# Performance work log

Measured on AMD Instinct MI355X. Metric: run time of the kernel, lower is better.

## Reference

```python
import jax, jax.numpy as jnp
import numpy as np

H = 1024
EPS = 1e-5
N_ENT = 1000
TOP_K = 5


def _ln(x, g, b):
    mu = jnp.mean(x, axis=-1, keepdims=True)
    var = jnp.mean((x - mu) ** 2, axis=-1, keepdims=True)
    return (x - mu) * jax.lax.rsqrt(var + EPS) * g + b


def _gelu(x):
    return jax.nn.gelu(x, approximate=False)  # torch nn.GELU default (erf)


def setup_inputs() -> dict:
    key = jax.random.key(0)
    ks = jax.random.split(key, 24)
    s = 0.02
    inp = {
        'hidden_states': jax.random.normal(ks[0], (8, 2048, H), jnp.float32),
        'entity_embeddings': jax.random.normal(ks[1], (N_ENT, H), jnp.float32) * 0.01,
        # entity_encoder: H -> 2H -> H -> LN
        'ee_w1': jax.random.normal(ks[2], (H, 2 * H), jnp.float32) * s,
        'ee_b1': jnp.zeros((2 * H,), jnp.float32),
        'ee_w2': jax.random.normal(ks[3], (2 * H, H), jnp.float32) * s,
        'ee_b2': jnp.zeros((H,), jnp.float32),
        'ee_g': jnp.ones((H,), jnp.float32),
        'ee_beta': jnp.zeros((H,), jnp.float32),
        # relation_encoder: H -> H -> H -> LN
        're_w1': jax.random.normal(ks[4], (H, H), jnp.float32) * s,
        're_b1': jnp.zeros((H,), jnp.float32),
        're_w2': jax.random.normal(ks[5], (H, H), jnp.float32) * s,
        're_b2': jnp.zeros((H,), jnp.float32),
        're_g': jnp.ones((H,), jnp.float32),
        're_beta': jnp.zeros((H,), jnp.float32),
        # reasoning_network: 3H -> 2H -> H -> LN
        'rn_w1': jax.random.normal(ks[6], (3 * H, 2 * H), jnp.float32) * s,
        'rn_b1': jnp.zeros((2 * H,), jnp.float32),
        'rn_w2': jax.random.normal(ks[7], (2 * H, H), jnp.float32) * s,
        'rn_b2': jnp.zeros((H,), jnp.float32),
        'rn_g': jnp.ones((H,), jnp.float32),
        'rn_beta': jnp.zeros((H,), jnp.float32),
        # validation_network: H -> H/2 -> 1 -> sigmoid
        'vn_w1': jax.random.normal(ks[8], (H, H // 2), jnp.float32) * s,
        'vn_b1': jnp.zeros((H // 2,), jnp.float32),
        'vn_w2': jax.random.normal(ks[9], (H // 2, 1), jnp.float32) * s,
        'vn_b2': jnp.zeros((1,), jnp.float32),
    }
    return inp


def reference(hidden_states, entity_embeddings,
              ee_w1, ee_b1, ee_w2, ee_b2, ee_g, ee_beta,
              re_w1, re_b1, re_w2, re_b2, re_g, re_beta,
              rn_w1, rn_b1, rn_w2, rn_b2, rn_g, rn_beta,
              vn_w1, vn_b1, vn_w2, vn_b2):
    # entity encoder over all tokens: [B,S,H]
    entity_features = _ln(_gelu(hidden_states @ ee_w1 + ee_b1) @ ee_w2 + ee_b2, ee_g, ee_beta)

    # query=None path: relation encoder on mean-pooled hidden states [B,H]
    pooled = jnp.mean(hidden_states, axis=1)
    relation_features = _ln(_gelu(pooled @ re_w1 + re_b1) @ re_w2 + re_b2, re_g, re_beta)
    query_features = relation_features

    # similarity + top-k entity retrieval
    entity_similarities = query_features @ entity_embeddings.T  # [B, N_ENT]
    top_values, top_indices = jax.lax.top_k(entity_similarities, TOP_K)
    retrieved_entities = entity_embeddings[top_indices]  # [B, K, H]

    # reasoning input: [mean retrieved entity | relation | mean context]
    entity_vec = jnp.mean(retrieved_entities, axis=1)  # [B,H]
    context_vec = jnp.mean(hidden_states, axis=1)      # [B,H]
    reasoning_in = jnp.concatenate([entity_vec, relation_features, context_vec], axis=-1)  # [B,3H]
    reasoning_output = _ln(_gelu(reasoning_in @ rn_w1 + rn_b1) @ rn_w2 + rn_b2, rn_g, rn_beta)

    validation_scores = jax.nn.sigmoid(_gelu(reasoning_output @ vn_w1 + vn_b1) @ vn_w2 + vn_b2)

    return (entity_features, relation_features, retrieved_entities,
            entity_similarities, top_indices, reasoning_output, validation_scores)
```

## Files before the change

### kernel.cpp

```cpp
#include <hip/hip_runtime.h>
#include <math.h>

#define H 1024
#define SEQ 2048
#define BATCH 8
#define N_ENT 1000
#define TOPK 5
#define LN_EPS 1e-5f

using bf16x8 = __attribute__((ext_vector_type(8))) __bf16;
using f32x4  = __attribute__((ext_vector_type(4))) float;
#define AS1 __attribute__((address_space(1)))
#define AS3 __attribute__((address_space(3)))


__device__ __forceinline__ float gelu_fast(float x) {
    float z = fabsf(x) * 0.70710678118654752440f;
    float t = __builtin_amdgcn_rcpf(fmaf(0.3275911f, z, 1.0f));
    float p = fmaf(fmaf(fmaf(fmaf(1.061405429f, t, -1.453152027f), t, 1.421413741f),
                        t, -0.284496736f), t, 0.254829592f) * t;
    float e = __builtin_amdgcn_exp2f(-z * z * 1.44269504088896f);
    float erfz = fmaf(-p, e, 1.0f);
    float s = copysignf(erfz, x);
    return 0.5f * x * (1.0f + s);
}

__device__ __forceinline__ float sigmoidf_(float x) {
    return 1.0f / (1.0f + expf(-x));
}

__device__ __forceinline__ unsigned short f2bf(float f) {
    unsigned int u = __float_as_uint(f);
    unsigned int r = (u + 0x7fffu + ((u >> 16) & 1u)) >> 16;
    return (unsigned short)r;
}

__device__ float block_sum(float v, float* red) {
    for (int off = 32; off > 0; off >>= 1) v += __shfl_down(v, off, 64);
    int wid = threadIdx.x >> 6;
    int lane = threadIdx.x & 63;
    int nw = blockDim.x >> 6;
    if (lane == 0) red[wid] = v;
    __syncthreads();
    if (threadIdx.x == 0) {
        float s = 0.f;
        for (int i = 0; i < nw; ++i) s += red[i];
        red[0] = s;
    }
    __syncthreads();
    float r = red[0];
    __syncthreads();
    return r;
}


__global__ void f2bf_kernel(const float* __restrict__ in, unsigned short* __restrict__ out, int n) {
    int i = (blockIdx.x * blockDim.x + threadIdx.x) * 4;
    if (i >= n) return;
    float4 v = *(const float4*)(in + i);
    ushort4 o;
    o.x = f2bf(v.x); o.y = f2bf(v.y); o.z = f2bf(v.z); o.w = f2bf(v.w);
    *(ushort4*)(out + i) = o;
}

__global__ void transpose_bf_kernel(const float* __restrict__ in, unsigned short* __restrict__ out,
                                    int R, int C) {
    __shared__ float tile[32][33];
    int c0 = blockIdx.x * 32, r0 = blockIdx.y * 32;
    int tx = threadIdx.x & 31, ty = threadIdx.x >> 5;
#pragma unroll
    for (int i = 0; i < 32; i += 8)
        tile[ty + i][tx] = in[(size_t)(r0 + ty + i) * C + c0 + tx];
    __syncthreads();
#pragma unroll
    for (int i = 0; i < 32; i += 8)
        out[(size_t)(c0 + ty + i) * R + r0 + tx] = f2bf(tile[tx][ty + i]);
}


__global__ void pool1_kernel(const float* __restrict__ hs, float* __restrict__ part,
                             unsigned short* __restrict__ hsb) {
    int sc = blockIdx.x, b = blockIdx.y, t = threadIdx.x;
    float a0 = 0, a1 = 0, a2 = 0, a3 = 0;
    size_t rowbase = (size_t)b * SEQ + sc * 64;
    const float* p = hs + rowbase * H;
    for (int s = 0; s < 64; ++s) {
        const float* q = p + (size_t)s * H;
        float v0 = q[t], v1 = q[t + 256], v2 = q[t + 512], v3 = q[t + 768];
        a0 += v0; a1 += v1; a2 += v2; a3 += v3;
        if (hsb) {
            unsigned short* w = hsb + (rowbase + s) * H;
            w[t] = f2bf(v0); w[t + 256] = f2bf(v1); w[t + 512] = f2bf(v2); w[t + 768] = f2bf(v3);
        }
    }
    float* o = part + ((size_t)b * 32 + sc) * H;
    o[t] = a0; o[t + 256] = a1; o[t + 512] = a2; o[t + 768] = a3;
}

__global__ void pool2_kernel(const float* __restrict__ part, float* __restrict__ pooled) {
    int b = blockIdx.y, c = blockIdx.x, t = threadIdx.x;
    float s = 0.f;
    for (int sc = 0; sc < 32; ++sc) s += part[((size_t)b * 32 + sc) * H + t + c * 256];
    pooled[b * H + t + c * 256] = s * (1.0f / SEQ);
}


template <int KRANGE>
__global__ void mlp_partial_kernel(const float* __restrict__ X, int ldx,
                                   const float* __restrict__ W, int N,
                                   float* __restrict__ part) {
    __shared__ float xs[8][KRANGE];
    int jb = blockIdx.x, ks = blockIdx.y, t = threadIdx.x;
    int k0 = ks * KRANGE;
    for (int i = t; i < 8 * KRANGE; i += 256) {
        int b = i / KRANGE, k = i % KRANGE;
        xs[b][k] = X[(size_t)b * ldx + k0 + k];
    }
    __syncthreads();
    int j = jb * 256 + t;
    float acc[8] = {};
    for (int k = 0; k < KRANGE; ++k) {
        float w = W[(size_t)(k0 + k) * N + j];
#pragma unroll
        for (int b = 0; b < 8; ++b) acc[b] = fmaf(xs[b][k], w, acc[b]);
    }
#pragma unroll
    for (int b = 0; b < 8; ++b) part[((size_t)ks * 8 + b) * N + j] = acc[b];
}

__global__ void mlp_reduce_gelu_kernel(const float* __restrict__ part, const float* __restrict__ bias,
                                       float* __restrict__ out, int N, int nks) {
    int b = blockIdx.y;
    int j = blockIdx.x * 256 + threadIdx.x;
    float s = bias[j];
    for (int ks = 0; ks < nks; ++ks) s += part[((size_t)ks * 8 + b) * N + j];
    out[(size_t)b * N + j] = gelu_fast(s);
}

__global__ void mlp_reduce_ln_kernel(const float* __restrict__ part, const float* __restrict__ bias,
                                     const float* __restrict__ g, const float* __restrict__ be,
                                     float* __restrict__ out, int nks) {
    __shared__ float red[32];
    int b = blockIdx.x, t = threadIdx.x;
    float s = bias[t];
    for (int ks = 0; ks < nks; ++ks) s += part[((size_t)ks * 8 + b) * H + t];
    float mu = block_sum(s, red) * (1.0f / H);
    float d = s - mu;
    float var = block_sum(d * d, red) * (1.0f / H);
    out[(size_t)b * H + t] = d * rsqrtf(var + LN_EPS) * g[t] + be[t];
}


__global__ void sim_kernel(const float* __restrict__ rel, const float* __restrict__ ent,
                           float* __restrict__ sims) {
    __shared__ float rl[8 * H];
    int t = threadIdx.x;
    for (int i = t; i < 8 * H; i += 256) rl[i] = rel[i];
    __syncthreads();
    int e = blockIdx.x * 4 + (t >> 6);
    int lane = t & 63;
    float ev[16];
    const float* ep = ent + (size_t)e * H;
#pragma unroll
    for (int i = 0; i < 16; ++i) ev[i] = ep[lane + i * 64];
#pragma unroll
    for (int b = 0; b < 8; ++b) {
        float a = 0.f;
#pragma unroll
        for (int i = 0; i < 16; ++i) a = fmaf(ev[i], rl[b * H + lane + i * 64], a);
        for (int off = 32; off > 0; off >>= 1) a += __shfl_down(a, off, 64);
        if (lane == 0) sims[b * N_ENT + e] = a;
    }
}

__global__ void topk_kernel(const float* __restrict__ sims, float* __restrict__ out_idx_f,
                            int* __restrict__ idx_i) {
    __shared__ float v[1024];
    __shared__ float rv[4];
    __shared__ int ri[4];
    int b = blockIdx.x, t = threadIdx.x;
    for (int i = t; i < 1024; i += 256) v[i] = (i < N_ENT) ? sims[b * N_ENT + i] : -INFINITY;
    __syncthreads();
    for (int k = 0; k < TOPK; ++k) {
        float best = -INFINITY;
        int bi = 0x7fffffff;
        for (int i = t; i < 1024; i += 256) {
            float x = v[i];
            if (x > best || (x == best && i < bi)) { best = x; bi = i; }
        }
        for (int off = 32; off > 0; off >>= 1) {
            float ov = __shfl_down(best, off, 64);
            int oi = __shfl_down(bi, off, 64);
            if (ov > best || (ov == best && oi < bi)) { best = ov; bi = oi; }
        }
        if ((t & 63) == 0) { rv[t >> 6] = best; ri[t >> 6] = bi; }
        __syncthreads();
        if (t == 0) {
            for (int w = 1; w < 4; ++w)
                if (rv[w] > rv[0] || (rv[w] == rv[0] && ri[w] < ri[0])) { rv[0] = rv[w]; ri[0] = ri[w]; }
            int sel = ri[0];
            out_idx_f[b * TOPK + k] = (float)sel;
            idx_i[b * TOPK + k] = sel;
            v[sel] = -INFINITY;
        }
        __syncthreads();
    }
}

__global__ void gather_concat_kernel(const float* __restrict__ ent, const int* __restrict__ idx,
                                     const float* __restrict__ rel, const float* __restrict__ pooled,
                                     float* __restrict__ retrieved, float* __restrict__ xin) {
    int b = blockIdx.x, h = threadIdx.x;
    float acc = 0.f;
    for (int k = 0; k < TOPK; ++k) {
        float v = ent[(size_t)idx[b * TOPK + k] * H + h];
        retrieved[((size_t)b * TOPK + k) * H + h] = v;
        acc += v;
    }
    float* xb = xin + (size_t)b * 3 * H;
    xb[h] = acc * (1.0f / TOPK);
    xb[H + h] = rel[b * H + h];
    xb[2 * H + h] = pooled[b * H + h];
}

__global__ void vn_final_kernel(const float* __restrict__ part, const float* __restrict__ b1,
                                const float* __restrict__ w2, const float* __restrict__ b2,
                                float* __restrict__ vs, int nks) {
    __shared__ float red[32];
    int b = blockIdx.x, t = threadIdx.x;
    float s = b1[t];
    for (int ks = 0; ks < nks; ++ks) s += part[((size_t)ks * 8 + b) * 512 + t];
    float c = gelu_fast(s) * w2[t];
    float tot = block_sum(c, red);
    if (t == 0) vs[b] = sigmoidf_(tot + b2[0]);
}

template <int GELU_BF16_OUT>
__global__ __launch_bounds__(256) void gemm_mfma(const unsigned short* __restrict__ A,
                                                 const unsigned short* __restrict__ Bt,
                                                 const float* __restrict__ bias,
                                                 void* __restrict__ Cout,
                                                 int M, int N, int K) {
    __shared__ __align__(16) unsigned short As[128 * 32];
    __shared__ __align__(16) unsigned short Bs[128 * 32];
    const int tid = threadIdx.x;
    const int lane = tid & 63;
    const int Mp = M >> 7;
    const int m0 = (blockIdx.x % Mp) * 128;
    const int n0 = (blockIdx.x / Mp) * 128;
    const int wave = tid >> 6;
    const int wm = (wave >> 1) * 64, wn = (wave & 1) * 64;

    const int rowA_f = wm + (lane & 15);
    const int rowB_f = wn + (lane & 15);
    const int kq = (lane >> 4) * 8;

    f32x4 acc[4][4] = {};

    for (int k0 = 0; k0 < K; k0 += 32) {
#pragma unroll
        for (int r = 0; r < 2; ++r) {
            int e = (r * 256 + tid) * 8;
            int row = e >> 5, kk = e & 31;
            const unsigned short* ga = A + (size_t)(m0 + row) * K + k0 + kk;
            const unsigned short* gb = Bt + (size_t)(n0 + row) * K + k0 + kk;
            unsigned short* la = As + (size_t)(r * 256 + (tid & ~63)) * 8;
            unsigned short* lb = Bs + (size_t)(r * 256 + (tid & ~63)) * 8;
            __builtin_amdgcn_global_load_lds((AS1 void*)ga, (AS3 void*)la, 16, 0, 0);
            __builtin_amdgcn_global_load_lds((AS1 void*)gb, (AS3 void*)lb, 16, 0, 0);
        }
        __syncthreads();
        bf16x8 af[4], bfg[4];
#pragma unroll
        for (int i = 0; i < 4; ++i)
            af[i] = *(const bf16x8*)(As + (rowA_f + i * 16) * 32 + kq);
#pragma unroll
        for (int j = 0; j < 4; ++j)
            bfg[j] = *(const bf16x8*)(Bs + (rowB_f + j * 16) * 32 + kq);
#pragma unroll
        for (int i = 0; i < 4; ++i)
#pragma unroll
            for (int j = 0; j < 4; ++j)
                acc[i][j] = __builtin_amdgcn_mfma_f32_16x16x32_bf16(af[i], bfg[j], acc[i][j], 0, 0, 0);
        __syncthreads();
    }

    const int cn = lane & 15;
    const int rbase = (lane >> 4) * 4;
#pragma unroll
    for (int i = 0; i < 4; ++i) {
#pragma unroll
        for (int j = 0; j < 4; ++j) {
            int n = n0 + wn + j * 16 + cn;
            float bv = bias[n];
            int mb = m0 + wm + i * 16 + rbase;
#pragma unroll
            for (int r = 0; r < 4; ++r) {
                float c = acc[i][j][r] + bv;
                if (GELU_BF16_OUT) {
                    c = gelu_fast(c);
                    ((unsigned short*)Cout)[(size_t)(mb + r) * N + n] = f2bf(c);
                } else {
                    ((float*)Cout)[(size_t)(mb + r) * N + n] = c;
                }
            }
        }
    }
}

__global__ void ln_rows_kernel(float* __restrict__ x, const float* __restrict__ g,
                               const float* __restrict__ beta) {
    __shared__ float red[32];
    float* p = x + (size_t)blockIdx.x * H;
    int t = threadIdx.x;
    float4 v = *(const float4*)(p + t * 4);
    float s = v.x + v.y + v.z + v.w;
    float mu = block_sum(s, red) * (1.0f / H);
    float4 d = { v.x - mu, v.y - mu, v.z - mu, v.w - mu };
    float d2 = d.x * d.x + d.y * d.y + d.z * d.z + d.w * d.w;
    float var = block_sum(d2, red) * (1.0f / H);
    float inv = rsqrtf(var + LN_EPS);
    float4 gg = *(const float4*)(g + t * 4);
    float4 bb = *(const float4*)(beta + t * 4);
    float4 o = { d.x * inv * gg.x + bb.x, d.y * inv * gg.y + bb.y,
                 d.z * inv * gg.z + bb.z, d.w * inv * gg.w + bb.w };
    *(float4*)(p + t * 4) = o;
}


extern "C" void kernel_launch(void* const* d_in, const int* in_sizes, int n_in,
                              void* d_out, int out_size, void* d_ws, size_t ws_size,
                              hipStream_t stream) {
    const float* hs     = (const float*)d_in[0];
    const float* ent    = (const float*)d_in[1];
    const float* ee_w1  = (const float*)d_in[2];
    const float* ee_b1  = (const float*)d_in[3];
    const float* ee_w2  = (const float*)d_in[4];
    const float* ee_b2  = (const float*)d_in[5];
    const float* ee_g   = (const float*)d_in[6];
    const float* ee_be  = (const float*)d_in[7];
    const float* re_w1  = (const float*)d_in[8];
    const float* re_b1  = (const float*)d_in[9];
    const float* re_w2  = (const float*)d_in[10];
    const float* re_b2  = (const float*)d_in[11];
    const float* re_g   = (const float*)d_in[12];
    const float* re_be  = (const float*)d_in[13];
    const float* rn_w1  = (const float*)d_in[14];
    const float* rn_b1  = (const float*)d_in[15];
    const float* rn_w2  = (const float*)d_in[16];
    const float* rn_b2  = (const float*)d_in[17];
    const float* rn_g   = (const float*)d_in[18];
    const float* rn_be  = (const float*)d_in[19];
    const float* vn_w1  = (const float*)d_in[20];
    const float* vn_b1  = (const float*)d_in[21];
    const float* vn_w2  = (const float*)d_in[22];
    const float* vn_b2  = (const float*)d_in[23];

    float* out = (float*)d_out;
    float* ef   = out;
    float* rel  = ef + (size_t)BATCH * SEQ * H;
    float* retr = rel + BATCH * H;
    float* sims = retr + BATCH * TOPK * H;
    float* tidx = sims + BATCH * N_ENT;
    float* ro   = tidx + BATCH * TOPK;
    float* vs   = ro + BATCH * H;

    float* ws = (float*)d_ws;
    size_t o = 0;
    float* pooled = ws + o; o += 8192;
    int*   idx_i  = (int*)(ws + o); o += 64;
    float* xin    = ws + o; o += 8 * 3 * H;
    float* h1r    = ws + o; o += 8 * H;
    float* h1n    = ws + o; o += 8 * 2 * H;
    float* part   = ws + o; o += 24 * 8 * 2048;
    unsigned short* w1t = (unsigned short*)(ws + o); o += (2048 * 1024) / 2;
    unsigned short* w2t = (unsigned short*)(ws + o); o += (2048 * 1024) / 2;
    unsigned short* hsb = (unsigned short*)(ws + o);

    long long avail = (long long)(ws_size / 4) - (long long)o;
    int chunk = (int)(avail / 1536);
    chunk &= ~127;
    int total = BATCH * SEQ;
    if (chunk > total) chunk = total;
    if (chunk < 128) chunk = 128;
    bool full = (chunk >= total);
    unsigned short* midb = hsb + (size_t)chunk * H;

    transpose_bf_kernel<<<dim3(2048 / 32, 1024 / 32), 256, 0, stream>>>(ee_w1, w1t, 1024, 2048);
    transpose_bf_kernel<<<dim3(1024 / 32, 2048 / 32), 256, 0, stream>>>(ee_w2, w2t, 2048, 1024);

    pool1_kernel<<<dim3(32, BATCH), 256, 0, stream>>>(hs, part, full ? hsb : nullptr);
    pool2_kernel<<<dim3(4, BATCH), 256, 0, stream>>>(part, pooled);

    mlp_partial_kernel<64><<<dim3(4, 16), 256, 0, stream>>>(pooled, H, re_w1, H, part);
    mlp_reduce_gelu_kernel<<<dim3(4, 8), 256, 0, stream>>>(part, re_b1, h1r, H, 16);
    mlp_partial_kernel<64><<<dim3(4, 16), 256, 0, stream>>>(h1r, H, re_w2, H, part);
    mlp_reduce_ln_kernel<<<BATCH, 1024, 0, stream>>>(part, re_b2, re_g, re_be, rel, 16);

    sim_kernel<<<250, 256, 0, stream>>>(rel, ent, sims);
    topk_kernel<<<BATCH, 256, 0, stream>>>(sims, tidx, idx_i);
    gather_concat_kernel<<<BATCH, 1024, 0, stream>>>(ent, idx_i, rel, pooled, retr, xin);

    mlp_partial_kernel<128><<<dim3(8, 24), 256, 0, stream>>>(xin, 3 * H, rn_w1, 2 * H, part);
    mlp_reduce_gelu_kernel<<<dim3(8, 8), 256, 0, stream>>>(part, rn_b1, h1n, 2 * H, 24);
    mlp_partial_kernel<128><<<dim3(4, 16), 256, 0, stream>>>(h1n, 2 * H, rn_w2, H, part);
    mlp_reduce_ln_kernel<<<BATCH, 1024, 0, stream>>>(part, rn_b2, rn_g, rn_be, ro, 16);

    mlp_partial_kernel<128><<<dim3(2, 8), 256, 0, stream>>>(ro, H, vn_w1, 512, part);
    vn_final_kernel<<<BATCH, 512, 0, stream>>>(part, vn_b1, vn_w2, vn_b2, vs, 8);

    for (int r0 = 0; r0 < total; r0 += chunk) {
        int m = total - r0;
        if (m > chunk) m = chunk;
        if (!full) {
            int nconv = m * H;
            f2bf_kernel<<<(nconv / 4 + 255) / 256, 256, 0, stream>>>(hs + (size_t)r0 * H, hsb, nconv);
        }
        unsigned short* a1 = full ? (hsb + (size_t)r0 * H) : hsb;
        gemm_mfma<1><<<(m / 128) * (2048 / 128), 256, 0, stream>>>(a1, w1t, ee_b1, midb,
                                                                   m, 2048, 1024);
        gemm_mfma<0><<<(m / 128) * (1024 / 128), 256, 0, stream>>>(midb, w2t, ee_b2,
                                                                   ef + (size_t)r0 * H,
                                                                   m, 1024, 2048);
    }
    ln_rows_kernel<<<total, 256, 0, stream>>>(ef, ee_g, ee_be);
}
```

Before: 617.7 us.

## Double-buffer MFMA GEMM LDS tiles, group tile order, fuse small MLP reductions

The bf16 MFMA GEMM now keeps two LDS buffers, so the next K-slice is loaded while MFMAs run on the current one, with one barrier per iteration instead of two. Output tiles are also ordered in groups of 8 M-tiles to improve L2 reuse of the weight tiles. Separately, the small batch-8 MLPs drop the split-K partial-plus-reduce kernels for a single fc_kernel that reduces within the block and applies bias and GELU directly. This cuts launches and partial-buffer traffic, but far fewer blocks stream the large weight matrices, which may lower bandwidth on those layers.

```diff
diff --git a/kernel.cpp b/kernel.cpp
--- a/kernel.cpp
+++ b/kernel.cpp
@@ -104,46 +104,45 @@
     pooled[b * H + t + c * 256] = s * (1.0f / SEQ);
 }
 
-
-template <int KRANGE>
-__global__ void mlp_partial_kernel(const float* __restrict__ X, int ldx,
-                                   const float* __restrict__ W, int N,
-                                   float* __restrict__ part) {
-    __shared__ float xs[8][KRANGE];
-    int jb = blockIdx.x, ks = blockIdx.y, t = threadIdx.x;
-    int k0 = ks * KRANGE;
-    for (int i = t; i < 8 * KRANGE; i += 256) {
-        int b = i / KRANGE, k = i % KRANGE;
-        xs[b][k] = X[(size_t)b * ldx + k0 + k];
-    }
-    __syncthreads();
-    int j = jb * 256 + t;
+template <int K, int ACT>
+__global__ __launch_bounds__(256) void fc_kernel(const float* __restrict__ X,
+                                                 const float* __restrict__ W,
+                                                 const float* __restrict__ bias, int N,
+                                                 float* __restrict__ out) {
+    __shared__ float xs[8 * K];
+    __shared__ float red[4][8][64];
+    int t = threadIdx.x;
+    for (int i = t; i < 8 * K; i += 256) xs[i] = X[i];
+    __syncthreads();
+    int cl = t & 63;
+    int c = blockIdx.x * 64 + cl;
+    int s = t >> 6;
+    const int KS = K / 4;
     float acc[8] = {};
-    for (int k = 0; k < KRANGE; ++k) {
-        float w = W[(size_t)(k0 + k) * N + j];
-#pragma unroll
-        for (int b = 0; b < 8; ++b) acc[b] = fmaf(xs[b][k], w, acc[b]);
-    }
-#pragma unroll
-    for (int b = 0; b < 8; ++b) part[((size_t)ks * 8 + b) * N + j] = acc[b];
-}
-
-__global__ void mlp_reduce_gelu_kernel(const float* __restrict__ part, const float* __restrict__ bias,
-                                       float* __restrict__ out, int N, int nks) {
-    int b = blockIdx.y;
-    int j = blockIdx.x * 256 + threadIdx.x;
-    float s = bias[j];
-    for (int ks = 0; ks < nks; ++ks) s += part[((size_t)ks * 8 + b) * N + j];
-    out[(size_t)b * N + j] = gelu_fast(s);
-}
-
-__global__ void mlp_reduce_ln_kernel(const float* __restrict__ part, const float* __restrict__ bias,
-                                     const float* __restrict__ g, const float* __restrict__ be,
-                                     float* __restrict__ out, int nks) {
+#pragma unroll 4
+    for (int k = s * KS; k < (s + 1) * KS; ++k) {
+        float w = W[(size_t)k * N + c];
+#pragma unroll
+        for (int b = 0; b < 8; ++b) acc[b] = fmaf(xs[b * K + k], w, acc[b]);
+    }
+#pragma unroll
+    for (int b = 0; b < 8; ++b) red[s][b][cl] = acc[b];
+    __syncthreads();
+    if (s == 0) {
+#pragma unroll
+        for (int b = 0; b < 8; ++b) {
+            float v = red[0][b][cl] + red[1][b][cl] + red[2][b][cl] + red[3][b][cl] + bias[c];
+            if (ACT) v = gelu_fast(v);
+            out[(size_t)b * N + c] = v;
+        }
+    }
+}
+
+__global__ void ln_vec_kernel(const float* __restrict__ in, const float* __restrict__ g,
+                              const float* __restrict__ be, float* __restrict__ out) {
     __shared__ float red[32];
     int b = blockIdx.x, t = threadIdx.x;
-    float s = bias[t];
-    for (int ks = 0; ks < nks; ++ks) s += part[((size_t)ks * 8 + b) * H + t];
+    float s = in[(size_t)b * H + t];
     float mu = block_sum(s, red) * (1.0f / H);
     float d = s - mu;
     float var = block_sum(d * d, red) * (1.0f / H);
@@ -223,14 +222,11 @@
     xb[2 * H + h] = pooled[b * H + h];
 }
 
-__global__ void vn_final_kernel(const float* __restrict__ part, const float* __restrict__ b1,
-                                const float* __restrict__ w2, const float* __restrict__ b2,
-                                float* __restrict__ vs, int nks) {
+__global__ void vn_final_kernel(const float* __restrict__ h, const float* __restrict__ w2,
+                                const float* __restrict__ b2, float* __restrict__ vs) {
     __shared__ float red[32];
     int b = blockIdx.x, t = threadIdx.x;
-    float s = b1[t];
-    for (int ks = 0; ks < nks; ++ks) s += part[((size_t)ks * 8 + b) * 512 + t];
-    float c = gelu_fast(s) * w2[t];
+    float c = h[(size_t)b * 512 + t] * w2[t];
     float tot = block_sum(c, red);
     if (t == 0) vs[b] = sigmoidf_(tot + b2[0]);
 }
@@ -241,48 +237,62 @@
                                                  const float* __restrict__ bias,
                                                  void* __restrict__ Cout,
                                                  int M, int N, int K) {
-    __shared__ __align__(16) unsigned short As[128 * 32];
-    __shared__ __align__(16) unsigned short Bs[128 * 32];
+    __shared__ __align__(16) unsigned short As[2][128 * 32];
+    __shared__ __align__(16) unsigned short Bs[2][128 * 32];
     const int tid = threadIdx.x;
     const int lane = tid & 63;
-    const int Mp = M >> 7;
-    const int m0 = (blockIdx.x % Mp) * 128;
-    const int n0 = (blockIdx.x / Mp) * 128;
+
+    const int Mp = M >> 7, Np = N >> 7;
+    const int GM = 8;
+    int per_group = GM * Np;
+    int group = blockIdx.x / per_group;
+    int rem = blockIdx.x - group * per_group;
+    int gbase = group * GM;
+    int gm = Mp - gbase; if (gm > GM) gm = GM;
+    const int m0 = (gbase + rem % gm) * 128;
+    const int n0 = (rem / gm) * 128;
+
     const int wave = tid >> 6;
     const int wm = (wave >> 1) * 64, wn = (wave & 1) * 64;
-
     const int rowA_f = wm + (lane & 15);
     const int rowB_f = wn + (lane & 15);
     const int kq = (lane >> 4) * 8;
 
-    f32x4 acc[4][4] = {};
-
-    for (int k0 = 0; k0 < K; k0 += 32) {
+    auto stage = [&](int kbase, int buf) {
 #pragma unroll
         for (int r = 0; r < 2; ++r) {
             int e = (r * 256 + tid) * 8;
             int row = e >> 5, kk = e & 31;
-            const unsigned short* ga = A + (size_t)(m0 + row) * K + k0 + kk;
-            const unsigned short* gb = Bt + (size_t)(n0 + row) * K + k0 + kk;
-            unsigned short* la = As + (size_t)(r * 256 + (tid & ~63)) * 8;
-            unsigned short* lb = Bs + (size_t)(r * 256 + (tid & ~63)) * 8;
+            const unsigned short* ga = A + (size_t)(m0 + row) * K + kbase + kk;
+            const unsigned short* gb = Bt + (size_t)(n0 + row) * K + kbase + kk;
+            unsigned short* la = &As[buf][(size_t)(r * 256 + (tid & ~63)) * 8];
+            unsigned short* lb = &Bs[buf][(size_t)(r * 256 + (tid & ~63)) * 8];
             __builtin_amdgcn_global_load_lds((AS1 void*)ga, (AS3 void*)la, 16, 0, 0);
             __builtin_amdgcn_global_load_lds((AS1 void*)gb, (AS3 void*)lb, 16, 0, 0);
         }
+    };
+
+    f32x4 acc[4][4] = {};
+    stage(0, 0);
+    int cur = 0;
+    for (int k0 = 0; k0 < K; k0 += 32) {
         __syncthreads();
+        if (k0 + 32 < K) stage(k0 + 32, cur ^ 1);
+        const unsigned short* Ab = As[cur];
+        const unsigned short* Bb = Bs[cur];
         bf16x8 af[4], bfg[4];
 #pragma unroll
         for (int i = 0; i < 4; ++i)
-            af[i] = *(const bf16x8*)(As + (rowA_f + i * 16) * 32 + kq);
+            af[i] = *(const bf16x8*)(Ab + (rowA_f + i * 16) * 32 + kq);
 #pragma unroll
         for (int j = 0; j < 4; ++j)
-            bfg[j] = *(const bf16x8*)(Bs + (rowB_f + j * 16) * 32 + kq);
+            bfg[j] = *(const bf16x8*)(Bb + (rowB_f + j * 16) * 32 + kq);
 #pragma unroll
         for (int i = 0; i < 4; ++i)
 #pragma unroll
             for (int j = 0; j < 4; ++j)
                 acc[i][j] = __builtin_amdgcn_mfma_f32_16x16x32_bf16(af[i], bfg[j], acc[i][j], 0, 0, 0);
-        __syncthreads();
+        cur ^= 1;
     }
 
     const int cn = lane & 15;
@@ -371,8 +381,11 @@
     int*   idx_i  = (int*)(ws + o); o += 64;
     float* xin    = ws + o; o += 8 * 3 * H;
     float* h1r    = ws + o; o += 8 * H;
+    float* relp   = ws + o; o += 8 * H;
     float* h1n    = ws + o; o += 8 * 2 * H;
-    float* part   = ws + o; o += 24 * 8 * 2048;
+    float* rop    = ws + o; o += 8 * H;
+    float* h1v    = ws + o; o += 8 * 512;
+    float* part   = ws + o; o += 8 * 32 * H;
     unsigned short* w1t = (unsigned short*)(ws + o); o += (2048 * 1024) / 2;
     unsigned short* w2t = (unsigned short*)(ws + o); o += (2048 * 1024) / 2;
     unsigned short* hsb = (unsigned short*)(ws + o);
@@ -392,22 +405,20 @@
     pool1_kernel<<<dim3(32, BATCH), 256, 0, stream>>>(hs, part, full ? hsb : nullptr);
     pool2_kernel<<<dim3(4, BATCH), 256, 0, stream>>>(part, pooled);
 
-    mlp_partial_kernel<64><<<dim3(4, 16), 256, 0, stream>>>(pooled, H, re_w1, H, part);
-    mlp_reduce_gelu_kernel<<<dim3(4, 8), 256, 0, stream>>>(part, re_b1, h1r, H, 16);
-    mlp_partial_kernel<64><<<dim3(4, 16), 256, 0, stream>>>(h1r, H, re_w2, H, part);
-    mlp_reduce_ln_kernel<<<BATCH, 1024, 0, stream>>>(part, re_b2, re_g, re_be, rel, 16);
+    fc_kernel<1024, 1><<<16, 256, 0, stream>>>(pooled, re_w1, re_b1, 1024, h1r);
+    fc_kernel<1024, 0><<<16, 256, 0, stream>>>(h1r, re_w2, re_b2, 1024, relp);
+    ln_vec_kernel<<<BATCH, 1024, 0, stream>>>(relp, re_g, re_be, rel);
 
     sim_kernel<<<250, 256, 0, stream>>>(rel, ent, sims);
     topk_kernel<<<BATCH, 256, 0, stream>>>(sims, tidx, idx_i);
     gather_concat_kernel<<<BATCH, 1024, 0, stream>>>(ent, idx_i, rel, pooled, retr, xin);
 
-    mlp_partial_kernel<128><<<dim3(8, 24), 256, 0, stream>>>(xin, 3 * H, rn_w1, 2 * H, part);
-    mlp_reduce_gelu_kernel<<<dim3(8, 8), 256, 0, stream>>>(part, rn_b1, h1n, 2 * H, 24);
-    mlp_partial_kernel<128><<<dim3(4, 16), 256, 0, stream>>>(h1n, 2 * H, rn_w2, H, part);
-    mlp_reduce_ln_kernel<<<BATCH, 1024, 0, stream>>>(part, rn_b2, rn_g, rn_be, ro, 16);
-
-    mlp_partial_kernel<128><<<dim3(2, 8), 256, 0, stream>>>(ro, H, vn_w1, 512, part);
-    vn_final_kernel<<<BATCH, 512, 0, stream>>>(part, vn_b1, vn_w2, vn_b2, vs, 8);
+    fc_kernel<3072, 1><<<32, 256, 0, stream>>>(xin, rn_w1, rn_b1, 2048, h1n);
+    fc_kernel<2048, 0><<<16, 256, 0, stream>>>(h1n, rn_w2, rn_b2, 1024, rop);
+    ln_vec_kernel<<<BATCH, 1024, 0, stream>>>(rop, rn_g, rn_be, ro);
+
+    fc_kernel<1024, 1><<<8, 256, 0, stream>>>(ro, vn_w1, vn_b1, 512, h1v);
+    vn_final_kernel<<<BATCH, 512, 0, stream>>>(h1v, vn_w2, vn_b2, vs);
 
     for (int r0 = 0; r0 < total; r0 += chunk) {
         int m = total - r0;
```

Measured after the change: 753.5 us. 1.22x slower.

## Double-buffer GEMM LDS tiles, add grouped block swizzle, vectorize pooling

Applied to the files above, without the earlier changes.

The MFMA GEMM now keeps two LDS buffers and issues the next K-tile's global-to-LDS loads before computing the current tile. This drops one barrier per iteration and overlaps memory with MFMA work. Blocks are remapped into groups of 8 M-tiles for better L2 reuse of B tiles. The pooling kernels switch to float4 loads and stores, and pool2 now launches one block per batch. The risks are twice the LDS per block, which can lower occupancy, and a possible race, since a single barrier per iteration may let the next prefetch overwrite a buffer other waves are still reading.

```diff
diff --git a/kernel.cpp b/kernel.cpp
--- a/kernel.cpp
+++ b/kernel.cpp
@@ -81,27 +81,30 @@
 __global__ void pool1_kernel(const float* __restrict__ hs, float* __restrict__ part,
                              unsigned short* __restrict__ hsb) {
     int sc = blockIdx.x, b = blockIdx.y, t = threadIdx.x;
-    float a0 = 0, a1 = 0, a2 = 0, a3 = 0;
     size_t rowbase = (size_t)b * SEQ + sc * 64;
-    const float* p = hs + rowbase * H;
+    const float* p = hs + rowbase * H + t * 4;
+    float4 a = {0.f, 0.f, 0.f, 0.f};
     for (int s = 0; s < 64; ++s) {
-        const float* q = p + (size_t)s * H;
-        float v0 = q[t], v1 = q[t + 256], v2 = q[t + 512], v3 = q[t + 768];
-        a0 += v0; a1 += v1; a2 += v2; a3 += v3;
+        float4 v = *(const float4*)(p + (size_t)s * H);
+        a.x += v.x; a.y += v.y; a.z += v.z; a.w += v.w;
         if (hsb) {
-            unsigned short* w = hsb + (rowbase + s) * H;
-            w[t] = f2bf(v0); w[t + 256] = f2bf(v1); w[t + 512] = f2bf(v2); w[t + 768] = f2bf(v3);
-        }
-    }
-    float* o = part + ((size_t)b * 32 + sc) * H;
-    o[t] = a0; o[t + 256] = a1; o[t + 512] = a2; o[t + 768] = a3;
+            ushort4 o;
+            o.x = f2bf(v.x); o.y = f2bf(v.y); o.z = f2bf(v.z); o.w = f2bf(v.w);
+            *(ushort4*)(hsb + (rowbase + s) * H + t * 4) = o;
+        }
+    }
+    *(float4*)(part + ((size_t)b * 32 + sc) * H + t * 4) = a;
 }
 
 __global__ void pool2_kernel(const float* __restrict__ part, float* __restrict__ pooled) {
-    int b = blockIdx.y, c = blockIdx.x, t = threadIdx.x;
-    float s = 0.f;
-    for (int sc = 0; sc < 32; ++sc) s += part[((size_t)b * 32 + sc) * H + t + c * 256];
-    pooled[b * H + t + c * 256] = s * (1.0f / SEQ);
+    int b = blockIdx.x, t = threadIdx.x;
+    float4 s = {0.f, 0.f, 0.f, 0.f};
+    for (int sc = 0; sc < 32; ++sc) {
+        float4 v = *(const float4*)(part + ((size_t)b * 32 + sc) * H + t * 4);
+        s.x += v.x; s.y += v.y; s.z += v.z; s.w += v.w;
+    }
+    float4 o = {s.x * (1.0f / SEQ), s.y * (1.0f / SEQ), s.z * (1.0f / SEQ), s.w * (1.0f / SEQ)};
+    *(float4*)(pooled + (size_t)b * H + t * 4) = o;
 }
 
 
@@ -241,48 +244,62 @@
                                                  const float* __restrict__ bias,
                                                  void* __restrict__ Cout,
                                                  int M, int N, int K) {
-    __shared__ __align__(16) unsigned short As[128 * 32];
-    __shared__ __align__(16) unsigned short Bs[128 * 32];
+    __shared__ __align__(16) unsigned short As[2][128 * 32];
+    __shared__ __align__(16) unsigned short Bs[2][128 * 32];
     const int tid = threadIdx.x;
     const int lane = tid & 63;
-    const int Mp = M >> 7;
-    const int m0 = (blockIdx.x % Mp) * 128;
-    const int n0 = (blockIdx.x / Mp) * 128;
+
+    const int Mp = M >> 7, Np = N >> 7;
+    const int GM = 8;
+    int per_group = GM * Np;
+    int group = blockIdx.x / per_group;
+    int rem = blockIdx.x - group * per_group;
+    int gbase = group * GM;
+    int gm = Mp - gbase; if (gm > GM) gm = GM;
+    const int m0 = (gbase + rem % gm) * 128;
+    const int n0 = (rem / gm) * 128;
+
     const int wave = tid >> 6;
     const int wm = (wave >> 1) * 64, wn = (wave & 1) * 64;
-
     const int rowA_f = wm + (lane & 15);
     const int rowB_f = wn + (lane & 15);
     const int kq = (lane >> 4) * 8;
 
-    f32x4 acc[4][4] = {};
-
-    for (int k0 = 0; k0 < K; k0 += 32) {
+    auto stage = [&](int kbase, int buf) {
 #pragma unroll
         for (int r = 0; r < 2; ++r) {
             int e = (r * 256 + tid) * 8;
             int row = e >> 5, kk = e & 31;
-            const unsigned short* ga = A + (size_t)(m0 + row) * K + k0 + kk;
-            const unsigned short* gb = Bt + (size_t)(n0 + row) * K + k0 + kk;
-            unsigned short* la = As + (size_t)(r * 256 + (tid & ~63)) * 8;
-            unsigned short* lb = Bs + (size_t)(r * 256 + (tid & ~63)) * 8;
+            const unsigned short* ga = A + (size_t)(m0 + row) * K + kbase + kk;
+            const unsigned short* gb = Bt + (size_t)(n0 + row) * K + kbase + kk;
+            unsigned short* la = &As[buf][(size_t)(r * 256 + (tid & ~63)) * 8];
+            unsigned short* lb = &Bs[buf][(size_t)(r * 256 + (tid & ~63)) * 8];
             __builtin_amdgcn_global_load_lds((AS1 void*)ga, (AS3 void*)la, 16, 0, 0);
             __builtin_amdgcn_global_load_lds((AS1 void*)gb, (AS3 void*)lb, 16, 0, 0);
         }
+    };
+
+    f32x4 acc[4][4] = {};
+    stage(0, 0);
+    int cur = 0;
+    for (int k0 = 0; k0 < K; k0 += 32) {
         __syncthreads();
+        if (k0 + 32 < K) stage(k0 + 32, cur ^ 1);
+        const unsigned short* Ab = As[cur];
+        const unsigned short* Bb = Bs[cur];
         bf16x8 af[4], bfg[4];
 #pragma unroll
         for (int i = 0; i < 4; ++i)
-            af[i] = *(const bf16x8*)(As + (rowA_f + i * 16) * 32 + kq);
+            af[i] = *(const bf16x8*)(Ab + (rowA_f + i * 16) * 32 + kq);
 #pragma unroll
         for (int j = 0; j < 4; ++j)
-            bfg[j] = *(const bf16x8*)(Bs + (rowB_f + j * 16) * 32 + kq);
+            bfg[j] = *(const bf16x8*)(Bb + (rowB_f + j * 16) * 32 + kq);
 #pragma unroll
         for (int i = 0; i < 4; ++i)
 #pragma unroll
             for (int j = 0; j < 4; ++j)
                 acc[i][j] = __builtin_amdgcn_mfma_f32_16x16x32_bf16(af[i], bfg[j], acc[i][j], 0, 0, 0);
-        __syncthreads();
+        cur ^= 1;
     }
 
     const int cn = lane & 15;
@@ -390,7 +407,7 @@
     transpose_bf_kernel<<<dim3(1024 / 32, 2048 / 32), 256, 0, stream>>>(ee_w2, w2t, 2048, 1024);
 
     pool1_kernel<<<dim3(32, BATCH), 256, 0, stream>>>(hs, part, full ? hsb : nullptr);
-    pool2_kernel<<<dim3(4, BATCH), 256, 0, stream>>>(part, pooled);
+    pool2_kernel<<<BATCH, 256, 0, stream>>>(part, pooled);
 
     mlp_partial_kernel<64><<<dim3(4, 16), 256, 0, stream>>>(pooled, H, re_w1, H, part);
     mlp_reduce_gelu_kernel<<<dim3(4, 8), 256, 0, stream>>>(part, re_b1, h1r, H, 16);
```

Result: faster. 577.6 us (-6.5%).
